# Performance work log

Measured on AMD Instinct MI355X. Metric: run time of the kernel, lower is better.

## Reference

```python
import jax, jax.numpy as jnp
import numpy as np

B, H, T, D, R = 2, 12, 2048, 64, 16
D_STD = D - R


def setup_inputs() -> dict:
    key = jax.random.key(0)
    ks = jax.random.split(key, 5)
    return {
        "Q": jax.random.normal(ks[0], (B, H, T, D), jnp.float32),
        "K": jax.random.normal(ks[1], (B, H, T, D), jnp.float32),
        "V": jax.random.normal(ks[2], (B, H, T, D), jnp.float32),
        "d_bias": jax.random.normal(ks[3], (B, H, T), jnp.float32),
        "W_recip": jax.random.normal(ks[4], (D, R), jnp.float32) * 0.02,
        "w_std": jnp.full((H,), 0.5, jnp.float32),
        "w_rec": jnp.full((H,), 0.3, jnp.float32),
        "w_disc": jnp.full((H,), 0.2, jnp.float32),
    }


def reference(Q, K, V, d_bias, W_recip, w_std, w_rec, w_disc):
    b, h, t, d = Q.shape
    r = W_recip.shape[1]
    d_std = d - r
    sq_std = jnp.sqrt(w_std)[None, :, None, None]  # [1,H,1,1]
    sq_rec = jnp.sqrt(w_rec)[None, :, None, None]
    Q_low = jnp.einsum("bhtd,dr->bhtr", Q, W_recip)  # [B,H,T,R]
    K_low = jnp.einsum("bhtd,dr->bhtr", K, W_recip)
    Q_aug = jnp.concatenate([sq_std * Q[..., :d_std], sq_rec * K_low], axis=-1)  # [B,H,T,D]
    K_aug = jnp.concatenate([sq_std * K[..., :d_std], sq_rec * Q_low], axis=-1)
    scale = 1.0 / jnp.sqrt(jnp.asarray(d, Q.dtype))
    scores = jnp.einsum("bhqd,bhkd->bhqk", Q_aug, K_aug) * scale  # [B,H,T,T]
    # rank-1 additive bias, broadcast over queries: bias[b,h,q,k] = w_disc[h]*d_bias[b,h,k]
    scores = scores + (w_disc[None, :, None, None] * d_bias[:, :, None, :])
    causal = jnp.tril(jnp.ones((t, t), bool))  # [T,T]
    scores = jnp.where(causal[None, None], scores, -jnp.inf)
    attn = jax.nn.softmax(scores, axis=-1)
    return jnp.einsum("bhqk,bhkd->bhqd", attn, V)
```

## Files before the change

kernel.cpp:

```cpp
#include <hip/hip_runtime.h>
#include <math.h>

#define T_SEQ 2048
#define NH    12
#define NB    2
#define BHC   (NB*NH)
#define NQT   32

typedef _Float16 half4_t __attribute__((ext_vector_type(4)));
typedef _Float16 half8_t __attribute__((ext_vector_type(8)));
typedef float    floatx4 __attribute__((ext_vector_type(4)));

__device__ __forceinline__ void async_cp16(const void* g, void* l) {
  __builtin_amdgcn_global_load_lds((const __attribute__((address_space(1))) void*)g,
                                   (__attribute__((address_space(3))) void*)l, 16, 0, 0);
}
__device__ __forceinline__ void async_cp4(const void* g, void* l) {
  __builtin_amdgcn_global_load_lds((const __attribute__((address_space(1))) void*)g,
                                   (__attribute__((address_space(3))) void*)l, 4, 0, 0);
}
__device__ __forceinline__ half8_t h8splat(_Float16 s) {
  return (half8_t){s, s, s, s, s, s, s, s};
}

__global__ __launch_bounds__(256) void prep_kernel(
    const float* __restrict__ Q, const float* __restrict__ K,
    const float* __restrict__ V, const float* __restrict__ W,
    const float* __restrict__ wstd, const float* __restrict__ wrec,
    ushort* __restrict__ QF, ushort* __restrict__ KF, ushort* __restrict__ VF)
{
  __shared__ __align__(16) _Float16 Qsh[64*72];
  __shared__ __align__(16) _Float16 Ksh[64*72];
  __shared__ __align__(16) _Float16 Vsh[64*72];
  __shared__ __align__(16) _Float16 Lqh[64*16];
  __shared__ __align__(16) _Float16 Lkh[64*16];

  const int tid = threadIdx.x;
  const int w = tid >> 6, lane = tid & 63;
  const int quad = lane >> 4, ln = lane & 15;
  const int bh = blockIdx.x >> 5, tblk = blockIdx.x & 31;
  const long g0 = ((long)bh * T_SEQ + tblk * 64) * 64;

  const float4* gQ = (const float4*)(Q + g0);
  const float4* gK = (const float4*)(K + g0);
  const float4* gV = (const float4*)(V + g0);
  for (int i = tid; i < 1024; i += 256) {
    int r = i >> 4, c4 = i & 15;
    float4 q = gQ[i], k = gK[i], v = gV[i];
    *(half4_t*)&Qsh[r*72 + c4*4] = (half4_t){(_Float16)q.x,(_Float16)q.y,(_Float16)q.z,(_Float16)q.w};
    *(half4_t*)&Ksh[r*72 + c4*4] = (half4_t){(_Float16)k.x,(_Float16)k.y,(_Float16)k.z,(_Float16)k.w};
    *(half4_t*)&Vsh[r*72 + c4*4] = (half4_t){(_Float16)v.x,(_Float16)v.y,(_Float16)v.z,(_Float16)v.w};
  }
  __syncthreads();

  half4_t bw[4];
#pragma unroll
  for (int dk = 0; dk < 4; dk++)
#pragma unroll
    for (int i = 0; i < 4; i++)
      bw[dk][i] = (_Float16)W[(dk*16 + quad*4 + i)*16 + ln];

  floatx4 cq = {0.f,0.f,0.f,0.f}, ck = {0.f,0.f,0.f,0.f};
#pragma unroll
  for (int dk = 0; dk < 4; dk++) {
    half4_t aq = *(const half4_t*)&Qsh[(w*16 + ln)*72 + dk*16 + quad*4];
    half4_t ak = *(const half4_t*)&Ksh[(w*16 + ln)*72 + dk*16 + quad*4];
    cq = __builtin_amdgcn_mfma_f32_16x16x16f16(aq, bw[dk], cq, 0, 0, 0);
    ck = __builtin_amdgcn_mfma_f32_16x16x16f16(ak, bw[dk], ck, 0, 0, 0);
  }
#pragma unroll
  for (int i = 0; i < 4; i++) {
    Lqh[(w*16 + quad*4 + i)*16 + ln] = (_Float16)cq[i];
    Lkh[(w*16 + quad*4 + i)*16 + ln] = (_Float16)ck[i];
  }
  __syncthreads();

  const int h = bh % NH;
  const float sstd = sqrtf(wstd[h]);
  const float srec = sqrtf(wrec[h]);
  const half8_t hq_std = h8splat((_Float16)(0.125f * sstd));
  const half8_t hk_std = h8splat((_Float16)sstd);
  const half8_t hq_rec = h8splat((_Float16)(0.125f * srec));
  const half8_t hk_rec = h8splat((_Float16)srec);

#pragma unroll
  for (int cc = 0; cc < 2; cc++) {
    int c = tid + cc * 256;
    {
      int lp = c & 63, dp = (c >> 6) & 1, rt = c >> 7;
      int row = rt*16 + (lp & 15);
      int d0 = dp*32 + (lp >> 4)*8;
      half8_t hq, hk;
      if (d0 < 48) {
        hq = *(const half8_t*)&Qsh[row*72 + d0] * hq_std;
        hk = *(const half8_t*)&Ksh[row*72 + d0] * hk_std;
      } else {
        hq = *(const half8_t*)&Lkh[row*16 + (d0-48)] * hq_rec;
        hk = *(const half8_t*)&Lqh[row*16 + (d0-48)] * hk_rec;
      }
      long tile16 = (long)bh*128 + tblk*4 + rt;
      ((int4*)QF)[tile16*128 + dp*64 + lp] = *(int4*)&hq;
      ((int4*)KF)[tile16*128 + dp*64 + lp] = *(int4*)&hk;
    }
    {
      int lv = c & 63, nt = (c >> 6) & 3, v2 = c >> 8;
      int d = nt*16 + (lv & 15), qv = lv >> 4;
      half8_t hv;
#pragma unroll
      for (int j = 0; j < 4; j++) {
        hv[j]   = Vsh[(v2*32 + qv*4 + j)*72 + d];
        hv[4+j] = Vsh[(v2*32 + 16 + qv*4 + j)*72 + d];
      }
      ((int4*)VF)[((long)bh*32 + tblk)*512 + (v2*4 + nt)*64 + lv] = *(int4*)&hv;
    }
  }
}

__global__ __launch_bounds__(256) void flash_kernel(
    const ushort* __restrict__ QF, const ushort* __restrict__ KF,
    const ushort* __restrict__ VF, const float* __restrict__ dbias,
    const float* __restrict__ wdisc, float* __restrict__ Out)
{
  __shared__ __align__(16) ushort KsL[2][4096];
  __shared__ __align__(16) ushort VsL[2][4096];
  __shared__ float bs[2][64];

  const int tid = threadIdx.x;
  const int w = tid >> 6, lane = tid & 63;
  const int quad = lane >> 4, ln = lane & 15;
  const int bid = blockIdx.x;
  const int bh = bid % BHC;
  const int qt = NQT - 1 - bid / BHC;
  const int h = bh % NH;
  const int q0 = qt * 64;
  const int qrow = q0 + w*16 + ln;
  const float wd = wdisc[h];

  const ushort* gKb = KF + ((long)bh*256) * 512;
  const ushort* gVb = VF + ((long)bh*256) * 512;
  const float*  gB  = dbias + (long)bh*T_SEQ;

  half8_t bq[2];
  {
    const ushort* gQ = QF + ((long)bh*128 + qt*4 + w) * 1024;
    bq[0] = *(const half8_t*)(gQ + lane*8);
    bq[1] = *(const half8_t*)(gQ + 512 + lane*8);
  }

  float m_i = -1e30f, l_i = 0.f;
  floatx4 acc[4];
#pragma unroll
  for (int nt = 0; nt < 4; nt++) acc[nt] = (floatx4){0.f,0.f,0.f,0.f};

  {
    for (int c = w; c < 8; c += 4) {
      async_cp16(gKb + c*512 + lane*8, &KsL[0][c*512]);
      async_cp16(gVb + c*512 + lane*8, &VsL[0][c*512]);
    }
    if (w == 0) async_cp4(gB + lane, &bs[0][0]);
  }

  for (int kt = 0; kt <= qt; kt++) {
    const int cur = kt & 1;
    __syncthreads();

    if (kt < qt) {
      const long o = (long)(kt + 1) * 8 * 512;
      for (int c = w; c < 8; c += 4) {
        async_cp16(gKb + o + c*512 + lane*8, &KsL[1-cur][c*512]);
        async_cp16(gVb + o + c*512 + lane*8, &VsL[1-cur][c*512]);
      }
      if (w == 0) async_cp4(gB + (kt+1)*64 + lane, &bs[1-cur][0]);
    }

    floatx4 st[4];
#pragma unroll
    for (int mt = 0; mt < 4; mt++) st[mt] = (floatx4){0.f,0.f,0.f,0.f};
#pragma unroll
    for (int mt = 0; mt < 4; mt++)
#pragma unroll
      for (int dp = 0; dp < 2; dp++) {
        half8_t a = *(const half8_t*)&KsL[cur][(mt*2 + dp)*512 + lane*8];
        st[mt] = __builtin_amdgcn_mfma_f32_16x16x32_f16(a, bq[dp], st[mt], 0, 0, 0);
      }

    const bool diag = (kt == qt);
    float rowmax = -1e30f;
#pragma unroll
    for (int mt = 0; mt < 4; mt++)
#pragma unroll
      for (int i = 0; i < 4; i++) {
        float v = st[mt][i] + wd * bs[cur][mt*16 + quad*4 + i];
        int key = kt*64 + mt*16 + quad*4 + i;
        if (diag && key > qrow) v = -1e30f;
        st[mt][i] = v;
        rowmax = fmaxf(rowmax, v);
      }
    rowmax = fmaxf(rowmax, __shfl_xor(rowmax, 16));
    rowmax = fmaxf(rowmax, __shfl_xor(rowmax, 32));
    float mnew  = fmaxf(m_i, rowmax);
    float alpha = __expf(m_i - mnew);
    float psum = 0.f;
    half4_t pa[4];
#pragma unroll
    for (int mt = 0; mt < 4; mt++)
#pragma unroll
      for (int i = 0; i < 4; i++) {
        float p = __expf(st[mt][i] - mnew);
        psum += p;
        pa[mt][i] = (_Float16)p;
      }
    psum += __shfl_xor(psum, 16);
    psum += __shfl_xor(psum, 32);
    l_i = l_i * alpha + psum;
    m_i = mnew;

    float af[4];
#pragma unroll
    for (int i = 0; i < 4; i++) af[i] = __shfl(alpha, quad*4 + i);
#pragma unroll
    for (int nt = 0; nt < 4; nt++)
#pragma unroll
      for (int i = 0; i < 4; i++) acc[nt][i] *= af[i];

#pragma unroll
    for (int v2 = 0; v2 < 2; v2++)
#pragma unroll
      for (int nt = 0; nt < 4; nt++) {
        half8_t vv = *(const half8_t*)&VsL[cur][(v2*4 + nt)*512 + lane*8];
        half4_t b0 = __builtin_shufflevector(vv, vv, 0,1,2,3);
        half4_t b1 = __builtin_shufflevector(vv, vv, 4,5,6,7);
        acc[nt] = __builtin_amdgcn_mfma_f32_16x16x16f16(pa[2*v2],   b0, acc[nt], 0, 0, 0);
        acc[nt] = __builtin_amdgcn_mfma_f32_16x16x16f16(pa[2*v2+1], b1, acc[nt], 0, 0, 0);
      }
  }

  float lr[4];
#pragma unroll
  for (int i = 0; i < 4; i++) lr[i] = 1.f / __shfl(l_i, quad*4 + i);
  const long obase = (long)bh*T_SEQ*64 + (long)(q0 + w*16)*64;
#pragma unroll
  for (int i = 0; i < 4; i++)
#pragma unroll
    for (int nt = 0; nt < 4; nt++)
      Out[obase + (quad*4 + i)*64 + nt*16 + ln] = acc[nt][i] * lr[i];
}

extern "C" void kernel_launch(void* const* d_in, const int* in_sizes, int n_in,
                              void* d_out, int out_size, void* d_ws, size_t ws_size,
                              hipStream_t stream) {
  const float* Q     = (const float*)d_in[0];
  const float* K     = (const float*)d_in[1];
  const float* V     = (const float*)d_in[2];
  const float* dbias = (const float*)d_in[3];
  const float* W     = (const float*)d_in[4];
  const float* wstd  = (const float*)d_in[5];
  const float* wrec  = (const float*)d_in[6];
  const float* wdisc = (const float*)d_in[7];
  float* Out = (float*)d_out;

  const long NEL = (long)BHC * T_SEQ * 64;
  ushort* QF = (ushort*)d_ws;
  ushort* KF = QF + NEL;
  ushort* VF = KF + NEL;

  prep_kernel<<<BHC * NQT, 256, 0, stream>>>(Q, K, V, W, wstd, wrec, QF, KF, VF);
  flash_kernel<<<BHC * NQT, 256, 0, stream>>>(QF, KF, VF, dbias, wdisc, Out);
}
```

Measured before the change: 142.0 us.

## Fuse prep and flash kernels into one cooperative launch with grid sync

Merges the preprocessing kernel and the flash-attention kernel into a single cooperative kernel separated by a grid-wide barrier, removing one kernel launch and the gap between them. To fit the 768-block grid co-resident (launch bounds of 3 blocks per CU), shared memory is unioned and the K/V double buffer is dropped, so each tile is now loaded synchronously between two barriers. This loses load/compute overlap in the attention loop and adds grid-sync cost, and it may fail to launch if occupancy does not allow all blocks to be resident.

```diff
diff --git a/kernel.cpp b/kernel.cpp
--- a/kernel.cpp
+++ b/kernel.cpp
@@ -1,5 +1,8 @@
 #include <hip/hip_runtime.h>
+#include <hip/hip_cooperative_groups.h>
 #include <math.h>
+
+namespace cg = cooperative_groups;
 
 #define T_SEQ 2048
 #define NH    12
@@ -23,227 +26,221 @@
   return (half8_t){s, s, s, s, s, s, s, s};
 }
 
-__global__ __launch_bounds__(256) void prep_kernel(
+__global__ __launch_bounds__(256, 3) void fused_kernel(
     const float* __restrict__ Q, const float* __restrict__ K,
-    const float* __restrict__ V, const float* __restrict__ W,
-    const float* __restrict__ wstd, const float* __restrict__ wrec,
-    ushort* __restrict__ QF, ushort* __restrict__ KF, ushort* __restrict__ VF)
+    const float* __restrict__ V, const float* __restrict__ dbias,
+    const float* __restrict__ W, const float* __restrict__ wstd,
+    const float* __restrict__ wrec, const float* __restrict__ wdisc,
+    ushort* __restrict__ QF, ushort* __restrict__ KF, ushort* __restrict__ VF,
+    float* __restrict__ Out)
 {
-  __shared__ __align__(16) _Float16 Qsh[64*72];
-  __shared__ __align__(16) _Float16 Ksh[64*72];
-  __shared__ __align__(16) _Float16 Vsh[64*72];
-  __shared__ __align__(16) _Float16 Lqh[64*16];
-  __shared__ __align__(16) _Float16 Lkh[64*16];
+  __shared__ __align__(16) char smem[31744];
 
   const int tid = threadIdx.x;
   const int w = tid >> 6, lane = tid & 63;
   const int quad = lane >> 4, ln = lane & 15;
-  const int bh = blockIdx.x >> 5, tblk = blockIdx.x & 31;
-  const long g0 = ((long)bh * T_SEQ + tblk * 64) * 64;
-
-  const float4* gQ = (const float4*)(Q + g0);
-  const float4* gK = (const float4*)(K + g0);
-  const float4* gV = (const float4*)(V + g0);
-  for (int i = tid; i < 1024; i += 256) {
-    int r = i >> 4, c4 = i & 15;
-    float4 q = gQ[i], k = gK[i], v = gV[i];
-    *(half4_t*)&Qsh[r*72 + c4*4] = (half4_t){(_Float16)q.x,(_Float16)q.y,(_Float16)q.z,(_Float16)q.w};
-    *(half4_t*)&Ksh[r*72 + c4*4] = (half4_t){(_Float16)k.x,(_Float16)k.y,(_Float16)k.z,(_Float16)k.w};
-    *(half4_t*)&Vsh[r*72 + c4*4] = (half4_t){(_Float16)v.x,(_Float16)v.y,(_Float16)v.z,(_Float16)v.w};
+
+  {
+    _Float16* Qsh = (_Float16*)smem;
+    _Float16* Ksh = (_Float16*)(smem + 9216);
+    _Float16* Vsh = (_Float16*)(smem + 18432);
+    _Float16* Lqh = (_Float16*)(smem + 27648);
+    _Float16* Lkh = (_Float16*)(smem + 29696);
+
+    const int bh = blockIdx.x >> 5, tblk = blockIdx.x & 31;
+    const long g0 = ((long)bh * T_SEQ + tblk * 64) * 64;
+
+    const float4* gQ = (const float4*)(Q + g0);
+    const float4* gK = (const float4*)(K + g0);
+    const float4* gV = (const float4*)(V + g0);
+    for (int i = tid; i < 1024; i += 256) {
+      int r = i >> 4, c4 = i & 15;
+      float4 q = gQ[i], k = gK[i], v = gV[i];
+      *(half4_t*)&Qsh[r*72 + c4*4] = (half4_t){(_Float16)q.x,(_Float16)q.y,(_Float16)q.z,(_Float16)q.w};
+      *(half4_t*)&Ksh[r*72 + c4*4] = (half4_t){(_Float16)k.x,(_Float16)k.y,(_Float16)k.z,(_Float16)k.w};
+      *(half4_t*)&Vsh[r*72 + c4*4] = (half4_t){(_Float16)v.x,(_Float16)v.y,(_Float16)v.z,(_Float16)v.w};
+    }
+    __syncthreads();
+
+    half4_t bw[4];
+#pragma unroll
+    for (int dk = 0; dk < 4; dk++)
+#pragma unroll
+      for (int i = 0; i < 4; i++)
+        bw[dk][i] = (_Float16)W[(dk*16 + quad*4 + i)*16 + ln];
+
+    floatx4 cq = {0.f,0.f,0.f,0.f}, ck = {0.f,0.f,0.f,0.f};
+#pragma unroll
+    for (int dk = 0; dk < 4; dk++) {
+      half4_t aq = *(const half4_t*)&Qsh[(w*16 + ln)*72 + dk*16 + quad*4];
+      half4_t ak = *(const half4_t*)&Ksh[(w*16 + ln)*72 + dk*16 + quad*4];
+      cq = __builtin_amdgcn_mfma_f32_16x16x16f16(aq, bw[dk], cq, 0, 0, 0);
+      ck = __builtin_amdgcn_mfma_f32_16x16x16f16(ak, bw[dk], ck, 0, 0, 0);
+    }
+#pragma unroll
+    for (int i = 0; i < 4; i++) {
+      Lqh[(w*16 + quad*4 + i)*16 + ln] = (_Float16)cq[i];
+      Lkh[(w*16 + quad*4 + i)*16 + ln] = (_Float16)ck[i];
+    }
+    __syncthreads();
+
+    const int h = bh % NH;
+    const float sstd = sqrtf(wstd[h]);
+    const float srec = sqrtf(wrec[h]);
+    const half8_t hq_std = h8splat((_Float16)(0.125f * sstd));
+    const half8_t hk_std = h8splat((_Float16)sstd);
+    const half8_t hq_rec = h8splat((_Float16)(0.125f * srec));
+    const half8_t hk_rec = h8splat((_Float16)srec);
+
+#pragma unroll
+    for (int cc = 0; cc < 2; cc++) {
+      int c = tid + cc * 256;
+      {
+        int lp = c & 63, dp = (c >> 6) & 1, rt = c >> 7;
+        int row = rt*16 + (lp & 15);
+        int d0 = dp*32 + (lp >> 4)*8;
+        half8_t hq, hk;
+        if (d0 < 48) {
+          hq = *(const half8_t*)&Qsh[row*72 + d0] * hq_std;
+          hk = *(const half8_t*)&Ksh[row*72 + d0] * hk_std;
+        } else {
+          hq = *(const half8_t*)&Lkh[row*16 + (d0-48)] * hq_rec;
+          hk = *(const half8_t*)&Lqh[row*16 + (d0-48)] * hk_rec;
+        }
+        long tile16 = (long)bh*128 + tblk*4 + rt;
+        ((int4*)QF)[tile16*128 + dp*64 + lp] = *(int4*)&hq;
+        ((int4*)KF)[tile16*128 + dp*64 + lp] = *(int4*)&hk;
+      }
+      {
+        int lv = c & 63, nt = (c >> 6) & 3, v2 = c >> 8;
+        int d = nt*16 + (lv & 15), qv = lv >> 4;
+        half8_t hv;
+#pragma unroll
+        for (int j = 0; j < 4; j++) {
+          hv[j]   = Vsh[(v2*32 + qv*4 + j)*72 + d];
+          hv[4+j] = Vsh[(v2*32 + 16 + qv*4 + j)*72 + d];
+        }
+        ((int4*)VF)[((long)bh*32 + tblk)*512 + (v2*4 + nt)*64 + lv] = *(int4*)&hv;
+      }
+    }
   }
-  __syncthreads();
-
-  half4_t bw[4];
-#pragma unroll
-  for (int dk = 0; dk < 4; dk++)
+
+  __threadfence();
+  cg::this_grid().sync();
+
+  {
+    ushort* KsL = (ushort*)smem;
+    ushort* VsL = (ushort*)(smem + 8192);
+    float*  bs  = (float*)(smem + 16384);
+
+    const int bid = blockIdx.x;
+    const int bh = bid % BHC;
+    const int qt = NQT - 1 - bid / BHC;
+    const int h = bh % NH;
+    const int q0 = qt * 64;
+    const int qrow = q0 + w*16 + ln;
+    const float wd = wdisc[h];
+
+    const ushort* gKb = KF + (long)bh * 131072;
+    const ushort* gVb = VF + (long)bh * 131072;
+    const float*  gB  = dbias + (long)bh * T_SEQ;
+
+    half8_t bq[2];
+    {
+      const ushort* gQ = QF + ((long)bh*128 + qt*4 + w) * 1024;
+      bq[0] = *(const half8_t*)(gQ + lane*8);
+      bq[1] = *(const half8_t*)(gQ + 512 + lane*8);
+    }
+
+    float m_i = -1e30f, l_i = 0.f;
+    floatx4 acc[4];
+#pragma unroll
+    for (int nt = 0; nt < 4; nt++) acc[nt] = (floatx4){0.f,0.f,0.f,0.f};
+
+    for (int kt = 0; kt <= qt; kt++) {
+      __syncthreads();
+      {
+        const long o = (long)kt * 4096;
+        for (int c = w; c < 8; c += 4) {
+          async_cp16(gKb + o + c*512 + lane*8, &KsL[c*512]);
+          async_cp16(gVb + o + c*512 + lane*8, &VsL[c*512]);
+        }
+        if (w == 0) async_cp4(gB + kt*64 + lane, bs);
+      }
+      __syncthreads();
+
+      floatx4 st[4];
+#pragma unroll
+      for (int mt = 0; mt < 4; mt++) st[mt] = (floatx4){0.f,0.f,0.f,0.f};
+#pragma unroll
+      for (int mt = 0; mt < 4; mt++)
+#pragma unroll
+        for (int dp = 0; dp < 2; dp++) {
+          half8_t a = *(const half8_t*)&KsL[(mt*2 + dp)*512 + lane*8];
+          st[mt] = __builtin_amdgcn_mfma_f32_16x16x32_f16(a, bq[dp], st[mt], 0, 0, 0);
+        }
+
+      const bool diag = (kt == qt);
+      float rowmax = -1e30f;
+#pragma unroll
+      for (int mt = 0; mt < 4; mt++)
+#pragma unroll
+        for (int i = 0; i < 4; i++) {
+          float v = st[mt][i] + wd * bs[mt*16 + quad*4 + i];
+          int key = kt*64 + mt*16 + quad*4 + i;
+          if (diag && key > qrow) v = -1e30f;
+          st[mt][i] = v;
+          rowmax = fmaxf(rowmax, v);
+        }
+      rowmax = fmaxf(rowmax, __shfl_xor(rowmax, 16));
+      rowmax = fmaxf(rowmax, __shfl_xor(rowmax, 32));
+      float mnew  = fmaxf(m_i, rowmax);
+      float alpha = __expf(m_i - mnew);
+      float psum = 0.f;
+      half4_t pa[4];
+#pragma unroll
+      for (int mt = 0; mt < 4; mt++)
+#pragma unroll
+        for (int i = 0; i < 4; i++) {
+          float p = __expf(st[mt][i] - mnew);
+          psum += p;
+          pa[mt][i] = (_Float16)p;
+        }
+      psum += __shfl_xor(psum, 16);
+      psum += __shfl_xor(psum, 32);
+      l_i = l_i * alpha + psum;
+      m_i = mnew;
+
+      float af[4];
+#pragma unroll
+      for (int i = 0; i < 4; i++) af[i] = __shfl(alpha, quad*4 + i);
+#pragma unroll
+      for (int nt = 0; nt < 4; nt++)
+#pragma unroll
+        for (int i = 0; i < 4; i++) acc[nt][i] *= af[i];
+
+#pragma unroll
+      for (int v2 = 0; v2 < 2; v2++)
+#pragma unroll
+        for (int nt = 0; nt < 4; nt++) {
+          half8_t vv = *(const half8_t*)&VsL[(v2*4 + nt)*512 + lane*8];
+          half4_t b0 = __builtin_shufflevector(vv, vv, 0,1,2,3);
+          half4_t b1 = __builtin_shufflevector(vv, vv, 4,5,6,7);
+          acc[nt] = __builtin_amdgcn_mfma_f32_16x16x16f16(pa[2*v2],   b0, acc[nt], 0, 0, 0);
+          acc[nt] = __builtin_amdgcn_mfma_f32_16x16x16f16(pa[2*v2+1], b1, acc[nt], 0, 0, 0);
+        }
+    }
+
+    float lr[4];
+#pragma unroll
+    for (int i = 0; i < 4; i++) lr[i] = 1.f / __shfl(l_i, quad*4 + i);
+    const long obase = (long)bh*T_SEQ*64 + (long)(q0 + w*16)*64;
 #pragma unroll
     for (int i = 0; i < 4; i++)
-      bw[dk][i] = (_Float16)W[(dk*16 + quad*4 + i)*16 + ln];
-
-  floatx4 cq = {0.f,0.f,0.f,0.f}, ck = {0.f,0.f,0.f,0.f};
-#pragma unroll
-  for (int dk = 0; dk < 4; dk++) {
-    half4_t aq = *(const half4_t*)&Qsh[(w*16 + ln)*72 + dk*16 + quad*4];
-    half4_t ak = *(const half4_t*)&Ksh[(w*16 + ln)*72 + dk*16 + quad*4];
-    cq = __builtin_amdgcn_mfma_f32_16x16x16f16(aq, bw[dk], cq, 0, 0, 0);
-    ck = __builtin_amdgcn_mfma_f32_16x16x16f16(ak, bw[dk], ck, 0, 0, 0);
+#pragma unroll
+      for (int nt = 0; nt < 4; nt++)
+        Out[obase + (quad*4 + i)*64 + nt*16 + ln] = acc[nt][i] * lr[i];
   }
-#pragma unroll
-  for (int i = 0; i < 4; i++) {
-    Lqh[(w*16 + quad*4 + i)*16 + ln] = (_Float16)cq[i];
-    Lkh[(w*16 + quad*4 + i)*16 + ln] = (_Float16)ck[i];
-  }
-  __syncthreads();
-
-  const int h = bh % NH;
-  const float sstd = sqrtf(wstd[h]);
-  const float srec = sqrtf(wrec[h]);
-  const half8_t hq_std = h8splat((_Float16)(0.125f * sstd));
-  const half8_t hk_std = h8splat((_Float16)sstd);
-  const half8_t hq_rec = h8splat((_Float16)(0.125f * srec));
-  const half8_t hk_rec = h8splat((_Float16)srec);
-
-#pragma unroll
-  for (int cc = 0; cc < 2; cc++) {
-    int c = tid + cc * 256;
-    {
-      int lp = c & 63, dp = (c >> 6) & 1, rt = c >> 7;
-      int row = rt*16 + (lp & 15);
-      int d0 = dp*32 + (lp >> 4)*8;
-      half8_t hq, hk;
-      if (d0 < 48) {
-        hq = *(const half8_t*)&Qsh[row*72 + d0] * hq_std;
-        hk = *(const half8_t*)&Ksh[row*72 + d0] * hk_std;
-      } else {
-        hq = *(const half8_t*)&Lkh[row*16 + (d0-48)] * hq_rec;
-        hk = *(const half8_t*)&Lqh[row*16 + (d0-48)] * hk_rec;
-      }
-      long tile16 = (long)bh*128 + tblk*4 + rt;
-      ((int4*)QF)[tile16*128 + dp*64 + lp] = *(int4*)&hq;
-      ((int4*)KF)[tile16*128 + dp*64 + lp] = *(int4*)&hk;
-    }
-    {
-      int lv = c & 63, nt = (c >> 6) & 3, v2 = c >> 8;
-      int d = nt*16 + (lv & 15), qv = lv >> 4;
-      half8_t hv;
-#pragma unroll
-      for (int j = 0; j < 4; j++) {
-        hv[j]   = Vsh[(v2*32 + qv*4 + j)*72 + d];
-        hv[4+j] = Vsh[(v2*32 + 16 + qv*4 + j)*72 + d];
-      }
-      ((int4*)VF)[((long)bh*32 + tblk)*512 + (v2*4 + nt)*64 + lv] = *(int4*)&hv;
-    }
-  }
-}
-
-__global__ __launch_bounds__(256) void flash_kernel(
-    const ushort* __restrict__ QF, const ushort* __restrict__ KF,
-    const ushort* __restrict__ VF, const float* __restrict__ dbias,
-    const float* __restrict__ wdisc, float* __restrict__ Out)
-{
-  __shared__ __align__(16) ushort KsL[2][4096];
-  __shared__ __align__(16) ushort VsL[2][4096];
-  __shared__ float bs[2][64];
-
-  const int tid = threadIdx.x;
-  const int w = tid >> 6, lane = tid & 63;
-  const int quad = lane >> 4, ln = lane & 15;
-  const int bid = blockIdx.x;
-  const int bh = bid % BHC;
-  const int qt = NQT - 1 - bid / BHC;
-  const int h = bh % NH;
-  const int q0 = qt * 64;
-  const int qrow = q0 + w*16 + ln;
-  const float wd = wdisc[h];
-
-  const ushort* gKb = KF + ((long)bh*256) * 512;
-  const ushort* gVb = VF + ((long)bh*256) * 512;
-  const float*  gB  = dbias + (long)bh*T_SEQ;
-
-  half8_t bq[2];
-  {
-    const ushort* gQ = QF + ((long)bh*128 + qt*4 + w) * 1024;
-    bq[0] = *(const half8_t*)(gQ + lane*8);
-    bq[1] = *(const half8_t*)(gQ + 512 + lane*8);
-  }
-
-  float m_i = -1e30f, l_i = 0.f;
-  floatx4 acc[4];
-#pragma unroll
-  for (int nt = 0; nt < 4; nt++) acc[nt] = (floatx4){0.f,0.f,0.f,0.f};
-
-  {
-    for (int c = w; c < 8; c += 4) {
-      async_cp16(gKb + c*512 + lane*8, &KsL[0][c*512]);
-      async_cp16(gVb + c*512 + lane*8, &VsL[0][c*512]);
-    }
-    if (w == 0) async_cp4(gB + lane, &bs[0][0]);
-  }
-
-  for (int kt = 0; kt <= qt; kt++) {
-    const int cur = kt & 1;
-    __syncthreads();
-
-    if (kt < qt) {
-      const long o = (long)(kt + 1) * 8 * 512;
-      for (int c = w; c < 8; c += 4) {
-        async_cp16(gKb + o + c*512 + lane*8, &KsL[1-cur][c*512]);
-        async_cp16(gVb + o + c*512 + lane*8, &VsL[1-cur][c*512]);
-      }
-      if (w == 0) async_cp4(gB + (kt+1)*64 + lane, &bs[1-cur][0]);
-    }
-
-    floatx4 st[4];
-#pragma unroll
-    for (int mt = 0; mt < 4; mt++) st[mt] = (floatx4){0.f,0.f,0.f,0.f};
-#pragma unroll
-    for (int mt = 0; mt < 4; mt++)
-#pragma unroll
-      for (int dp = 0; dp < 2; dp++) {
-        half8_t a = *(const half8_t*)&KsL[cur][(mt*2 + dp)*512 + lane*8];
-        st[mt] = __builtin_amdgcn_mfma_f32_16x16x32_f16(a, bq[dp], st[mt], 0, 0, 0);
-      }
-
-    const bool diag = (kt == qt);
-    float rowmax = -1e30f;
-#pragma unroll
-    for (int mt = 0; mt < 4; mt++)
-#pragma unroll
-      for (int i = 0; i < 4; i++) {
-        float v = st[mt][i] + wd * bs[cur][mt*16 + quad*4 + i];
-        int key = kt*64 + mt*16 + quad*4 + i;
-        if (diag && key > qrow) v = -1e30f;
-        st[mt][i] = v;
-        rowmax = fmaxf(rowmax, v);
-      }
-    rowmax = fmaxf(rowmax, __shfl_xor(rowmax, 16));
-    rowmax = fmaxf(rowmax, __shfl_xor(rowmax, 32));
-    float mnew  = fmaxf(m_i, rowmax);
-    float alpha = __expf(m_i - mnew);
-    float psum = 0.f;
-    half4_t pa[4];
-#pragma unroll
-    for (int mt = 0; mt < 4; mt++)
-#pragma unroll
-      for (int i = 0; i < 4; i++) {
-        float p = __expf(st[mt][i] - mnew);
-        psum += p;
-        pa[mt][i] = (_Float16)p;
-      }
-    psum += __shfl_xor(psum, 16);
-    psum += __shfl_xor(psum, 32);
-    l_i = l_i * alpha + psum;
-    m_i = mnew;
-
-    float af[4];
-#pragma unroll
-    for (int i = 0; i < 4; i++) af[i] = __shfl(alpha, quad*4 + i);
-#pragma unroll
-    for (int nt = 0; nt < 4; nt++)
-#pragma unroll
-      for (int i = 0; i < 4; i++) acc[nt][i] *= af[i];
-
-#pragma unroll
-    for (int v2 = 0; v2 < 2; v2++)
-#pragma unroll
-      for (int nt = 0; nt < 4; nt++) {
-        half8_t vv = *(const half8_t*)&VsL[cur][(v2*4 + nt)*512 + lane*8];
-        half4_t b0 = __builtin_shufflevector(vv, vv, 0,1,2,3);
-        half4_t b1 = __builtin_shufflevector(vv, vv, 4,5,6,7);
-        acc[nt] = __builtin_amdgcn_mfma_f32_16x16x16f16(pa[2*v2],   b0, acc[nt], 0, 0, 0);
-        acc[nt] = __builtin_amdgcn_mfma_f32_16x16x16f16(pa[2*v2+1], b1, acc[nt], 0, 0, 0);
-      }
-  }
-
-  float lr[4];
-#pragma unroll
-  for (int i = 0; i < 4; i++) lr[i] = 1.f / __shfl(l_i, quad*4 + i);
-  const long obase = (long)bh*T_SEQ*64 + (long)(q0 + w*16)*64;
-#pragma unroll
-  for (int i = 0; i < 4; i++)
-#pragma unroll
-    for (int nt = 0; nt < 4; nt++)
-      Out[obase + (quad*4 + i)*64 + nt*16 + ln] = acc[nt][i] * lr[i];
 }
 
 extern "C" void kernel_launch(void* const* d_in, const int* in_sizes, int n_in,
@@ -264,6 +261,9 @@
   ushort* KF = QF + NEL;
   ushort* VF = KF + NEL;
 
-  prep_kernel<<<BHC * NQT, 256, 0, stream>>>(Q, K, V, W, wstd, wrec, QF, KF, VF);
-  flash_kernel<<<BHC * NQT, 256, 0, stream>>>(QF, KF, VF, dbias, wdisc, Out);
-}
+  void* args[] = { (void*)&Q, (void*)&K, (void*)&V, (void*)&dbias, (void*)&W,
+                   (void*)&wstd, (void*)&wrec, (void*)&wdisc,
+                   (void*)&QF, (void*)&KF, (void*)&VF, (void*)&Out };
+  hipLaunchCooperativeKernel((const void*)fused_kernel, dim3(BHC * NQT), dim3(256),
+                             args, 0, stream);
+}
```

New measurement: 289.8 us. 104% more time.

## Replace double-buffered prefetch with paired-tile synchronous load per iteration

Applied to the files above, without the earlier changes.

Replaces the ping-pong async prefetch of one K/V tile ahead with a scheme that loads two consecutive K/V/bias tiles into shared memory, synchronizes, and then processes both tiles. This halves the number of barrier phases per key tile. In exchange, loads are no longer overlapped with the softmax and MFMA work of the previous tile, so memory latency is exposed unless other resident blocks hide it.

```diff
diff --git a/kernel.cpp b/kernel.cpp
--- a/kernel.cpp
+++ b/kernel.cpp
@@ -121,9 +121,9 @@
     const ushort* __restrict__ VF, const float* __restrict__ dbias,
     const float* __restrict__ wdisc, float* __restrict__ Out)
 {
-  __shared__ __align__(16) ushort KsL[2][4096];
-  __shared__ __align__(16) ushort VsL[2][4096];
-  __shared__ float bs[2][64];
+  __shared__ __align__(16) ushort KsL[8192];
+  __shared__ __align__(16) ushort VsL[8192];
+  __shared__ float bs[128];
 
   const int tid = threadIdx.x;
   const int w = tid >> 6, lane = tid & 63;
@@ -136,9 +136,9 @@
   const int qrow = q0 + w*16 + ln;
   const float wd = wdisc[h];
 
-  const ushort* gKb = KF + ((long)bh*256) * 512;
-  const ushort* gVb = VF + ((long)bh*256) * 512;
-  const float*  gB  = dbias + (long)bh*T_SEQ;
+  const ushort* gKb = KF + (long)bh * 131072;
+  const ushort* gVb = VF + (long)bh * 131072;
+  const float*  gB  = dbias + (long)bh * T_SEQ;
 
   half8_t bq[2];
   {
@@ -152,87 +152,87 @@
 #pragma unroll
   for (int nt = 0; nt < 4; nt++) acc[nt] = (floatx4){0.f,0.f,0.f,0.f};
 
-  {
-    for (int c = w; c < 8; c += 4) {
-      async_cp16(gKb + c*512 + lane*8, &KsL[0][c*512]);
-      async_cp16(gVb + c*512 + lane*8, &VsL[0][c*512]);
-    }
-    if (w == 0) async_cp4(gB + lane, &bs[0][0]);
-  }
-
-  for (int kt = 0; kt <= qt; kt++) {
-    const int cur = kt & 1;
+  for (int kt0 = 0; kt0 <= qt; kt0 += 2) {
     __syncthreads();
-
-    if (kt < qt) {
-      const long o = (long)(kt + 1) * 8 * 512;
-      for (int c = w; c < 8; c += 4) {
-        async_cp16(gKb + o + c*512 + lane*8, &KsL[1-cur][c*512]);
-        async_cp16(gVb + o + c*512 + lane*8, &VsL[1-cur][c*512]);
+    {
+      const long o = (long)kt0 * 4096;
+      for (int c = w; c < 16; c += 4) {
+        async_cp16(gKb + o + c*512 + lane*8, &KsL[c*512]);
+        async_cp16(gVb + o + c*512 + lane*8, &VsL[c*512]);
       }
-      if (w == 0) async_cp4(gB + (kt+1)*64 + lane, &bs[1-cur][0]);
-    }
-
-    floatx4 st[4];
-#pragma unroll
-    for (int mt = 0; mt < 4; mt++) st[mt] = (floatx4){0.f,0.f,0.f,0.f};
-#pragma unroll
-    for (int mt = 0; mt < 4; mt++)
-#pragma unroll
-      for (int dp = 0; dp < 2; dp++) {
-        half8_t a = *(const half8_t*)&KsL[cur][(mt*2 + dp)*512 + lane*8];
-        st[mt] = __builtin_amdgcn_mfma_f32_16x16x32_f16(a, bq[dp], st[mt], 0, 0, 0);
-      }
-
-    const bool diag = (kt == qt);
-    float rowmax = -1e30f;
-#pragma unroll
-    for (int mt = 0; mt < 4; mt++)
-#pragma unroll
-      for (int i = 0; i < 4; i++) {
-        float v = st[mt][i] + wd * bs[cur][mt*16 + quad*4 + i];
-        int key = kt*64 + mt*16 + quad*4 + i;
-        if (diag && key > qrow) v = -1e30f;
-        st[mt][i] = v;
-        rowmax = fmaxf(rowmax, v);
-      }
-    rowmax = fmaxf(rowmax, __shfl_xor(rowmax, 16));
-    rowmax = fmaxf(rowmax, __shfl_xor(rowmax, 32));
-    float mnew  = fmaxf(m_i, rowmax);
-    float alpha = __expf(m_i - mnew);
-    float psum = 0.f;
-    half4_t pa[4];
-#pragma unroll
-    for (int mt = 0; mt < 4; mt++)
-#pragma unroll
-      for (int i = 0; i < 4; i++) {
-        float p = __expf(st[mt][i] - mnew);
-        psum += p;
-        pa[mt][i] = (_Float16)p;
-      }
-    psum += __shfl_xor(psum, 16);
-    psum += __shfl_xor(psum, 32);
-    l_i = l_i * alpha + psum;
-    m_i = mnew;
-
-    float af[4];
-#pragma unroll
-    for (int i = 0; i < 4; i++) af[i] = __shfl(alpha, quad*4 + i);
-#pragma unroll
-    for (int nt = 0; nt < 4; nt++)
-#pragma unroll
-      for (int i = 0; i < 4; i++) acc[nt][i] *= af[i];
-
-#pragma unroll
-    for (int v2 = 0; v2 < 2; v2++)
-#pragma unroll
-      for (int nt = 0; nt < 4; nt++) {
-        half8_t vv = *(const half8_t*)&VsL[cur][(v2*4 + nt)*512 + lane*8];
-        half4_t b0 = __builtin_shufflevector(vv, vv, 0,1,2,3);
-        half4_t b1 = __builtin_shufflevector(vv, vv, 4,5,6,7);
-        acc[nt] = __builtin_amdgcn_mfma_f32_16x16x16f16(pa[2*v2],   b0, acc[nt], 0, 0, 0);
-        acc[nt] = __builtin_amdgcn_mfma_f32_16x16x16f16(pa[2*v2+1], b1, acc[nt], 0, 0, 0);
-      }
+      if (w < 2) async_cp4(gB + kt0*64 + w*64 + lane, &bs[w*64]);
+    }
+    __syncthreads();
+
+#pragma unroll
+    for (int t2 = 0; t2 < 2; t2++) {
+      const int kt = kt0 + t2;
+      if (kt > qt) break;
+      const ushort* Kt = &KsL[t2 * 4096];
+      const ushort* Vt = &VsL[t2 * 4096];
+      const float*  bt = &bs[t2 * 64];
+
+      floatx4 st[4];
+#pragma unroll
+      for (int mt = 0; mt < 4; mt++) st[mt] = (floatx4){0.f,0.f,0.f,0.f};
+#pragma unroll
+      for (int mt = 0; mt < 4; mt++)
+#pragma unroll
+        for (int dp = 0; dp < 2; dp++) {
+          half8_t a = *(const half8_t*)&Kt[(mt*2 + dp)*512 + lane*8];
+          st[mt] = __builtin_amdgcn_mfma_f32_16x16x32_f16(a, bq[dp], st[mt], 0, 0, 0);
+        }
+
+      const bool diag = (kt == qt);
+      float rowmax = -1e30f;
+#pragma unroll
+      for (int mt = 0; mt < 4; mt++)
+#pragma unroll
+        for (int i = 0; i < 4; i++) {
+          float v = st[mt][i] + wd * bt[mt*16 + quad*4 + i];
+          int key = kt*64 + mt*16 + quad*4 + i;
+          if (diag && key > qrow) v = -1e30f;
+          st[mt][i] = v;
+          rowmax = fmaxf(rowmax, v);
+        }
+      rowmax = fmaxf(rowmax, __shfl_xor(rowmax, 16));
+      rowmax = fmaxf(rowmax, __shfl_xor(rowmax, 32));
+      float mnew  = fmaxf(m_i, rowmax);
+      float alpha = __expf(m_i - mnew);
+      float psum = 0.f;
+      half4_t pa[4];
+#pragma unroll
+      for (int mt = 0; mt < 4; mt++)
+#pragma unroll
+        for (int i = 0; i < 4; i++) {
+          float p = __expf(st[mt][i] - mnew);
+          psum += p;
+          pa[mt][i] = (_Float16)p;
+        }
+      psum += __shfl_xor(psum, 16);
+      psum += __shfl_xor(psum, 32);
+      l_i = l_i * alpha + psum;
+      m_i = mnew;
+
+      float af[4];
+#pragma unroll
+      for (int i = 0; i < 4; i++) af[i] = __shfl(alpha, quad*4 + i);
+#pragma unroll
+      for (int nt = 0; nt < 4; nt++)
+#pragma unroll
+        for (int i = 0; i < 4; i++) acc[nt][i] *= af[i];
+
+#pragma unroll
+      for (int v2 = 0; v2 < 2; v2++)
+#pragma unroll
+        for (int nt = 0; nt < 4; nt++) {
+          half8_t vv = *(const half8_t*)&Vt[(v2*4 + nt)*512 + lane*8];
+          half4_t b0 = __builtin_shufflevector(vv, vv, 0,1,2,3);
+          half4_t b1 = __builtin_shufflevector(vv, vv, 4,5,6,7);
+          acc[nt] = __builtin_amdgcn_mfma_f32_16x16x16f16(pa[2*v2],   b0, acc[nt], 0, 0, 0);
+          acc[nt] = __builtin_amdgcn_mfma_f32_16x16x16f16(pa[2*v2+1], b1, acc[nt], 0, 0, 0);
+        }
+    }
   }
 
   float lr[4];
```

Result: faster. 136.7 us (-3.7%).

## Split flash attention into single-wave blocks per 16-row query tile, drop LDS staging

Applied to the files above, without the earlier changes.

The flash kernel now launches one 64-thread wavefront per 16-query tile, four times as many blocks, instead of four waves sharing a 64-query tile. K/V fragments are read straight from global memory (relying on L2/cache) rather than being double-buffered through LDS with async copies and barriers. The bias scaled by w_disc is precomputed in the prep kernel into a workspace buffer. This removes LDS traffic and __syncthreads and gives finer causal load balance, but each wave re-reads K/V tiles from global memory with no sharing between waves.

```diff
diff --git a/kernel.cpp b/kernel.cpp
--- a/kernel.cpp
+++ b/kernel.cpp
@@ -11,14 +11,6 @@
 typedef _Float16 half8_t __attribute__((ext_vector_type(8)));
 typedef float    floatx4 __attribute__((ext_vector_type(4)));
 
-__device__ __forceinline__ void async_cp16(const void* g, void* l) {
-  __builtin_amdgcn_global_load_lds((const __attribute__((address_space(1))) void*)g,
-                                   (__attribute__((address_space(3))) void*)l, 16, 0, 0);
-}
-__device__ __forceinline__ void async_cp4(const void* g, void* l) {
-  __builtin_amdgcn_global_load_lds((const __attribute__((address_space(1))) void*)g,
-                                   (__attribute__((address_space(3))) void*)l, 4, 0, 0);
-}
 __device__ __forceinline__ half8_t h8splat(_Float16 s) {
   return (half8_t){s, s, s, s, s, s, s, s};
 }
@@ -27,7 +19,9 @@
     const float* __restrict__ Q, const float* __restrict__ K,
     const float* __restrict__ V, const float* __restrict__ W,
     const float* __restrict__ wstd, const float* __restrict__ wrec,
-    ushort* __restrict__ QF, ushort* __restrict__ KF, ushort* __restrict__ VF)
+    const float* __restrict__ dbias, const float* __restrict__ wdisc,
+    ushort* __restrict__ QF, ushort* __restrict__ KF, ushort* __restrict__ VF,
+    float* __restrict__ B2)
 {
   __shared__ __align__(16) _Float16 Qsh[64*72];
   __shared__ __align__(16) _Float16 Ksh[64*72];
@@ -82,6 +76,9 @@
   const half8_t hk_std = h8splat((_Float16)sstd);
   const half8_t hq_rec = h8splat((_Float16)(0.125f * srec));
   const half8_t hk_rec = h8splat((_Float16)srec);
+
+  if (tid < 64) B2[(long)bh*T_SEQ + tblk*64 + tid] =
+      wdisc[h] * dbias[(long)bh*T_SEQ + tblk*64 + tid];
 
 #pragma unroll
   for (int cc = 0; cc < 2; cc++) {
@@ -116,33 +113,26 @@
   }
 }
 
-__global__ __launch_bounds__(256) void flash_kernel(
+__global__ __launch_bounds__(64, 4) void flash_kernel(
     const ushort* __restrict__ QF, const ushort* __restrict__ KF,
-    const ushort* __restrict__ VF, const float* __restrict__ dbias,
-    const float* __restrict__ wdisc, float* __restrict__ Out)
+    const ushort* __restrict__ VF, const float* __restrict__ B2,
+    float* __restrict__ Out)
 {
-  __shared__ __align__(16) ushort KsL[2][4096];
-  __shared__ __align__(16) ushort VsL[2][4096];
-  __shared__ float bs[2][64];
-
-  const int tid = threadIdx.x;
-  const int w = tid >> 6, lane = tid & 63;
+  const int lane = threadIdx.x;
   const int quad = lane >> 4, ln = lane & 15;
   const int bid = blockIdx.x;
-  const int bh = bid % BHC;
-  const int qt = NQT - 1 - bid / BHC;
-  const int h = bh % NH;
-  const int q0 = qt * 64;
-  const int qrow = q0 + w*16 + ln;
-  const float wd = wdisc[h];
-
-  const ushort* gKb = KF + ((long)bh*256) * 512;
-  const ushort* gVb = VF + ((long)bh*256) * 512;
-  const float*  gB  = dbias + (long)bh*T_SEQ;
+  const int bh  = bid % BHC;
+  const int t16 = 127 - bid / BHC;
+  const int qrow = t16*16 + ln;
+  const int ktmax = t16 >> 2;
+
+  const ushort* gK = KF + (long)bh * 131072;
+  const ushort* gV = VF + (long)bh * 131072;
+  const float*  gB = B2 + (long)bh * T_SEQ;
 
   half8_t bq[2];
   {
-    const ushort* gQ = QF + ((long)bh*128 + qt*4 + w) * 1024;
+    const ushort* gQ = QF + ((long)bh*128 + t16) * 1024;
     bq[0] = *(const half8_t*)(gQ + lane*8);
     bq[1] = *(const half8_t*)(gQ + 512 + lane*8);
   }
@@ -152,50 +142,36 @@
 #pragma unroll
   for (int nt = 0; nt < 4; nt++) acc[nt] = (floatx4){0.f,0.f,0.f,0.f};
 
-  {
-    for (int c = w; c < 8; c += 4) {
-      async_cp16(gKb + c*512 + lane*8, &KsL[0][c*512]);
-      async_cp16(gVb + c*512 + lane*8, &VsL[0][c*512]);
-    }
-    if (w == 0) async_cp4(gB + lane, &bs[0][0]);
-  }
-
-  for (int kt = 0; kt <= qt; kt++) {
-    const int cur = kt & 1;
-    __syncthreads();
-
-    if (kt < qt) {
-      const long o = (long)(kt + 1) * 8 * 512;
-      for (int c = w; c < 8; c += 4) {
-        async_cp16(gKb + o + c*512 + lane*8, &KsL[1-cur][c*512]);
-        async_cp16(gVb + o + c*512 + lane*8, &VsL[1-cur][c*512]);
-      }
-      if (w == 0) async_cp4(gB + (kt+1)*64 + lane, &bs[1-cur][0]);
-    }
+  for (int kt = 0; kt <= ktmax; kt++) {
+    const ushort* Kt = gK + (long)kt * 4096;
+    const ushort* Vt = gV + (long)kt * 4096;
 
     floatx4 st[4];
 #pragma unroll
-    for (int mt = 0; mt < 4; mt++) st[mt] = (floatx4){0.f,0.f,0.f,0.f};
-#pragma unroll
-    for (int mt = 0; mt < 4; mt++)
-#pragma unroll
-      for (int dp = 0; dp < 2; dp++) {
-        half8_t a = *(const half8_t*)&KsL[cur][(mt*2 + dp)*512 + lane*8];
-        st[mt] = __builtin_amdgcn_mfma_f32_16x16x32_f16(a, bq[dp], st[mt], 0, 0, 0);
-      }
-
-    const bool diag = (kt == qt);
+    for (int mt = 0; mt < 4; mt++) {
+      half8_t a0 = *(const half8_t*)(Kt + (mt*2    )*512 + lane*8);
+      half8_t a1 = *(const half8_t*)(Kt + (mt*2 + 1)*512 + lane*8);
+      floatx4 c = (floatx4){0.f,0.f,0.f,0.f};
+      c = __builtin_amdgcn_mfma_f32_16x16x32_f16(a0, bq[0], c, 0, 0, 0);
+      c = __builtin_amdgcn_mfma_f32_16x16x32_f16(a1, bq[1], c, 0, 0, 0);
+      st[mt] = c;
+    }
+
+    const bool diag = (kt == ktmax);
     float rowmax = -1e30f;
 #pragma unroll
-    for (int mt = 0; mt < 4; mt++)
+    for (int mt = 0; mt < 4; mt++) {
+      float4 bb = *(const float4*)(gB + kt*64 + mt*16 + quad*4);
+      float bv[4] = {bb.x, bb.y, bb.z, bb.w};
 #pragma unroll
       for (int i = 0; i < 4; i++) {
-        float v = st[mt][i] + wd * bs[cur][mt*16 + quad*4 + i];
+        float v = st[mt][i] + bv[i];
         int key = kt*64 + mt*16 + quad*4 + i;
         if (diag && key > qrow) v = -1e30f;
         st[mt][i] = v;
         rowmax = fmaxf(rowmax, v);
       }
+    }
     rowmax = fmaxf(rowmax, __shfl_xor(rowmax, 16));
     rowmax = fmaxf(rowmax, __shfl_xor(rowmax, 32));
     float mnew  = fmaxf(m_i, rowmax);
@@ -227,7 +203,7 @@
     for (int v2 = 0; v2 < 2; v2++)
 #pragma unroll
       for (int nt = 0; nt < 4; nt++) {
-        half8_t vv = *(const half8_t*)&VsL[cur][(v2*4 + nt)*512 + lane*8];
+        half8_t vv = *(const half8_t*)(Vt + (v2*4 + nt)*512 + lane*8);
         half4_t b0 = __builtin_shufflevector(vv, vv, 0,1,2,3);
         half4_t b1 = __builtin_shufflevector(vv, vv, 4,5,6,7);
         acc[nt] = __builtin_amdgcn_mfma_f32_16x16x16f16(pa[2*v2],   b0, acc[nt], 0, 0, 0);
@@ -238,7 +214,7 @@
   float lr[4];
 #pragma unroll
   for (int i = 0; i < 4; i++) lr[i] = 1.f / __shfl(l_i, quad*4 + i);
-  const long obase = (long)bh*T_SEQ*64 + (long)(q0 + w*16)*64;
+  const long obase = (long)bh*T_SEQ*64 + (long)(t16*16)*64;
 #pragma unroll
   for (int i = 0; i < 4; i++)
 #pragma unroll
@@ -263,7 +239,9 @@
   ushort* QF = (ushort*)d_ws;
   ushort* KF = QF + NEL;
   ushort* VF = KF + NEL;
-
-  prep_kernel<<<BHC * NQT, 256, 0, stream>>>(Q, K, V, W, wstd, wrec, QF, KF, VF);
-  flash_kernel<<<BHC * NQT, 256, 0, stream>>>(QF, KF, VF, dbias, wdisc, Out);
-}
+  float*  B2 = (float*)(VF + NEL);
+
+  prep_kernel<<<BHC * NQT, 256, 0, stream>>>(Q, K, V, W, wstd, wrec, dbias, wdisc,
+                                             QF, KF, VF, B2);
+  flash_kernel<<<BHC * 128, 64, 0, stream>>>(QF, KF, VF, B2, Out);
+}
```

Result: faster. 135.3 us (-4.7%).
